# Kernel optimization log

Hardware: AMD Instinct MI355X
Metric: run time of the kernel (lower is better)

## Reference

```python
import jax, jax.numpy as jnp
import numpy as np

B, T_SRC, T_TGT = 2048, 32, 32
D = 512            # d_model
D_SRC, D_TGT = 100, 80
L = 2              # n_layers


def setup_inputs() -> dict:
    key = jax.random.key(0)
    ks = jax.random.split(key, 16)
    s = 1.0 / float(np.sqrt(D))  # torch LSTM init scale
    u = lambda k, shape: jax.random.uniform(k, shape, jnp.float32, -s, s)
    return {
        "src": jax.random.randint(ks[0], (B, T_SRC), 0, D_SRC, dtype=jnp.int32),
        "tgt": jax.random.randint(ks[1], (B, T_TGT), 0, D_TGT, dtype=jnp.int32),
        "enc_emb": jax.random.normal(ks[2], (D_SRC, D), jnp.float32),
        "dec_emb": jax.random.normal(ks[3], (D_TGT, D), jnp.float32),
        "enc_Wih": u(ks[4], (L, 4 * D, D)),
        "enc_Whh": u(ks[5], (L, 4 * D, D)),
        "enc_bih": u(ks[6], (L, 4 * D)),
        "enc_bhh": u(ks[7], (L, 4 * D)),
        "dec_Wih": u(ks[8], (L, 4 * D, D)),
        "dec_Whh": u(ks[9], (L, 4 * D, D)),
        "dec_bih": u(ks[10], (L, 4 * D)),
        "dec_bhh": u(ks[11], (L, 4 * D)),
        "post_W": u(ks[12], (D_TGT, D)),
        "post_b": u(ks[13], (D_TGT,)),
    }


def lstm_cell(x, h, c, Wih, Whh, bih, bhh):
    # PyTorch gate order: i, f, g, o
    gates = x @ Wih.T + bih + h @ Whh.T + bhh  # [B, 4D]
    i, f, g, o = jnp.split(gates, 4, axis=-1)
    c_new = jax.nn.sigmoid(f) * c + jax.nn.sigmoid(i) * jnp.tanh(g)
    h_new = jax.nn.sigmoid(o) * jnp.tanh(c_new)
    return h_new, c_new


def reference(src, tgt, enc_emb, dec_emb, enc_Wih, enc_Whh, enc_bih, enc_bhh,
              dec_Wih, dec_Whh, dec_bih, dec_bhh, post_W, post_b):
    # Eval-mode forward: dropout = identity, teacher forcing disabled
    # (tf = random() < ratio AND self.training is False at inference).
    n_layers = enc_Wih.shape[0]
    Bb = src.shape[0]
    Dm = enc_emb.shape[1]

    # ---- encoder: multi-layer LSTM over src embeddings ----
    x = enc_emb[src].swapaxes(0, 1)  # [T_src, B, D]
    hs, cs = [], []
    z = jnp.zeros((Bb, Dm), x.dtype)
    for l in range(n_layers):
        def step(carry, xt, l=l):
            h, c = carry
            h, c = lstm_cell(xt, h, c, enc_Wih[l], enc_Whh[l], enc_bih[l], enc_bhh[l])
            return (h, c), h
        (hT, cT), x = jax.lax.scan(step, (z, z), x)
        hs.append(hT)
        cs.append(cT)
    h0 = jnp.stack(hs)  # [L, B, D]
    c0 = jnp.stack(cs)  # [L, B, D]

    prev0 = dec_emb[tgt[:, 0]]  # [B, D]

    def dec_step(carry, _):
        h, c, prev = carry
        x = prev
        new_h, new_c = [], []
        for l in range(n_layers):
            hl, cl = lstm_cell(x, h[l], c[l], dec_Wih[l], dec_Whh[l], dec_bih[l], dec_bhh[l])
            new_h.append(hl)
            new_c.append(cl)
            x = hl
        logits = x @ post_W.T + post_b          # [B, d_tgt]
        pred = jnp.argmax(logits, axis=-1)       # [B]
        prev = dec_emb[pred]                     # [B, D]
        return (jnp.stack(new_h), jnp.stack(new_c), prev), logits

    _, out = jax.lax.scan(dec_step, (h0, c0, prev0), None, length=tgt.shape[1])
    return out.swapaxes(0, 1)  # [B, T_tgt, d_tgt]
```

## Files before the change

### kernel.cpp

```cpp
#include <hip/hip_runtime.h>
#include <hip/hip_bf16.h>

#define B_  2048
#define T_  32
#define D_  512
#define G_  2048
#define VT_ 80
#define BD  (B_ * D_)
#define LWE ((size_t)G_ * D_)

typedef _Float16 half8 __attribute__((ext_vector_type(8)));
typedef _Float16 half4_t __attribute__((ext_vector_type(4)));
typedef float    f32x4 __attribute__((ext_vector_type(4)));

static __device__ __forceinline__ float sigm(float x) {
    return 1.0f / (1.0f + expf(-x));
}

__global__ void zero_ws(int4* __restrict__ p, int n) {
    int i = blockIdx.x * blockDim.x + threadIdx.x;
    if (i < n) p[i] = int4{0, 0, 0, 0};
}
__global__ void init_pred(const int* __restrict__ tgt, int* __restrict__ pred) {
    int i = blockIdx.x * blockDim.x + threadIdx.x;
    if (i < B_) pred[i] = tgt[i * T_];
}

__global__ void split_weights(const float* __restrict__ s0, const float* __restrict__ s1,
                              const float* __restrict__ s2, const float* __restrict__ s3,
                              const float* __restrict__ s4, const float* __restrict__ s5,
                              _Float16* __restrict__ Wbase) {
    int g = blockIdx.x * blockDim.x + threadIdx.x;
    int mat = g >> 17;
    int rem = g & 131071;
    int np  = rem >> 6;
    int kq  = rem & 63;
    const float* src = (mat == 0) ? s0 : (mat == 1) ? s1 : (mat == 2) ? s2
                     : (mat == 3) ? s3 : (mat == 4) ? s4 : s5;
    int n = (np & 3) * D_ + (np >> 2);
    const float* sp = src + (size_t)n * D_ + kq * 8;
    float4 v0 = ((const float4*)sp)[0], v1 = ((const float4*)sp)[1];
    float x[8] = {v0.x, v0.y, v0.z, v0.w, v1.x, v1.y, v1.z, v1.w};
    _Float16 hi[8], lo[8];
    #pragma unroll
    for (int u = 0; u < 8; ++u) {
        hi[u] = (_Float16)x[u];
        lo[u] = (_Float16)(x[u] - (float)hi[u]);
    }
    int tile = (np >> 4) * 16 + (kq >> 2);
    int lane = (np & 15) | ((kq & 3) << 4);
    size_t e = (size_t)tile * 512 + (size_t)lane * 8;
    _Float16* Whi = Wbase + (size_t)mat * (2 * LWE);
    _Float16* Wlo = Whi + LWE;
    *(half8*)(Whi + e) = *(half8*)hi;
    *(half8*)(Wlo + e) = *(half8*)lo;
}

__global__ void split_postW(const float* __restrict__ pw,
                            _Float16* __restrict__ Ph, _Float16* __restrict__ Pl) {
    int g = blockIdx.x * blockDim.x + threadIdx.x;
    if (g >= VT_ * 64) return;
    int v = g >> 6, kq = g & 63;
    const float* sp = pw + (size_t)v * D_ + kq * 8;
    float4 v0 = ((const float4*)sp)[0], v1 = ((const float4*)sp)[1];
    float x[8] = {v0.x, v0.y, v0.z, v0.w, v1.x, v1.y, v1.z, v1.w};
    _Float16 hi[8], lo[8];
    #pragma unroll
    for (int u = 0; u < 8; ++u) {
        hi[u] = (_Float16)x[u];
        lo[u] = (_Float16)(x[u] - (float)hi[u]);
    }
    int tile = (v >> 4) * 16 + (kq >> 2);
    int lane = (v & 15) | ((kq & 3) << 4);
    size_t e = (size_t)tile * 512 + (size_t)lane * 8;
    *(half8*)(Ph + e) = *(half8*)hi;
    *(half8*)(Pl + e) = *(half8*)lo;
}

__global__ void perm_bias(const float* __restrict__ ebih, const float* __restrict__ ebhh,
                          const float* __restrict__ dbih, const float* __restrict__ dbhh,
                          float* __restrict__ biasP) {
    int i = blockIdx.x * blockDim.x + threadIdx.x;
    int cfg = i >> 11, np = i & 2047;
    int n = (np & 3) * D_ + (np >> 2);
    const float* bi = ((cfg < 2) ? ebih : dbih) + (cfg & 1) * G_;
    const float* bh = ((cfg < 2) ? ebhh : dbhh) + (cfg & 1) * G_;
    biasP[cfg * G_ + np] = bi[n] + bh[n];
}

__global__ __launch_bounds__(256) void compute_P(
    const float* __restrict__ enc_emb, const float* __restrict__ dec_emb,
    const float* __restrict__ encW0,   const float* __restrict__ decW0,
    float* __restrict__ P) {
    __shared__ float es[10][D_];
    __shared__ float part[4][64][10];
    int by = blockIdx.y;
    bool enc = (by < 10);
    int r0 = enc ? by * 10 : 100 + (by - 10) * 10;
    int s0 = enc ? by * 10 : (by - 10) * 10;
    const float* emb = enc ? enc_emb : dec_emb;
    const float* W   = enc ? encW0 : decW0;
    int tid = threadIdx.x;
    #pragma unroll
    for (int it = 0; it < 5; ++it) {
        int i4 = it * 256 + tid;
        int rr = i4 >> 7, cc = i4 & 127;
        ((float4*)es[rr])[cc] = ((const float4*)(emb + (size_t)(s0 + rr) * D_))[cc];
    }
    __syncthreads();
    int o   = tid & 63;
    int seg = tid >> 6;
    int np = blockIdx.x * 64 + o;
    int n = (np & 3) * D_ + (np >> 2);
    const float* wr = W + (size_t)n * D_ + seg * 128;
    float acc[10];
    #pragma unroll
    for (int rr = 0; rr < 10; ++rr) acc[rr] = 0.f;
    for (int k = 0; k < 128; k += 4) {
        float4 w4 = *(const float4*)(wr + k);
        int kb = seg * 128 + k;
        #pragma unroll
        for (int rr = 0; rr < 10; ++rr)
            acc[rr] += es[rr][kb] * w4.x + es[rr][kb+1] * w4.y
                     + es[rr][kb+2] * w4.z + es[rr][kb+3] * w4.w;
    }
    #pragma unroll
    for (int rr = 0; rr < 10; ++rr) part[seg][o][rr] = acc[rr];
    __syncthreads();
    for (int i = tid; i < 640; i += 256) {
        int o2 = i & 63, rr = i >> 6;
        P[(size_t)(r0 + rr) * G_ + blockIdx.x * 64 + o2] =
            (part[0][o2][rr] + part[1][o2][rr]) + (part[2][o2][rr] + part[3][o2][rr]);
    }
}

static __device__ __forceinline__ void load_chunk(
    const _Float16* __restrict__ Ah, const _Float16* __restrict__ Al,
    const _Float16* __restrict__ Wh, const _Float16* __restrict__ Wl,
    int afr, int wfr, int kc, int lane, half8* A8, half8* B8) {
    size_t lo8 = (size_t)lane * 8;
    #pragma unroll
    for (int i = 0; i < 4; ++i) {
        size_t off = (((size_t)(afr + i) * 16 + kc) << 9) + lo8;
        A8[i]     = *(const half8*)(Ah + off);
        A8[4 + i] = *(const half8*)(Al + off);
    }
    #pragma unroll
    for (int j = 0; j < 4; ++j) {
        size_t off = (((size_t)(wfr + j) * 16 + kc) << 9) + lo8;
        B8[j]     = *(const half8*)(Wh + off);
        B8[4 + j] = *(const half8*)(Wl + off);
    }
}
static __device__ __forceinline__ void mfma_chunk(
    const half8* A8, const half8* B8, f32x4 acc[4][4]) {
    #pragma unroll
    for (int i = 0; i < 4; ++i)
        #pragma unroll
        for (int j = 0; j < 4; ++j) {
            acc[i][j] = __builtin_amdgcn_mfma_f32_16x16x32_f16(A8[i], B8[j], acc[i][j], 0, 0, 0);
            acc[i][j] = __builtin_amdgcn_mfma_f32_16x16x32_f16(A8[i], B8[4 + j], acc[i][j], 0, 0, 0);
            acc[i][j] = __builtin_amdgcn_mfma_f32_16x16x32_f16(A8[4 + i], B8[j], acc[i][j], 0, 0, 0);
        }
}

struct CellJob {
    const _Float16 *a0h, *a0l, *w0h, *w0l;
    int kclo0, kchi0;
    const _Float16 *a1h, *a1l, *w1h, *w1l;
    int kclo1, kchi1;
    const float *biasP;
    const float *P;
    const int  *idx;
    int idx_stride, emb_rows;
    float *c_io;
    _Float16 *hh_out, *hl_out;
};

__global__ __launch_bounds__(512, 2) void lstm_cell_mfma(CellJob J0, CellJob J1) {
    const CellJob J = (blockIdx.z == 0) ? J0 : J1;
    __shared__ float gf[128][68];
    const int tid  = threadIdx.x;
    const int w    = tid >> 6;
    const int lane = tid & 63;
    const int g    = w >> 2;
    const int mw   = w & 3;
    const int id   = blockIdx.x;
    const int bx   = id >> 3;
    const int m0   = (id & 7) * 256;

    const _Float16* Ah = g ? J.a1h : J.a0h;
    const _Float16* Al = g ? J.a1l : J.a0l;
    const _Float16* Wh = g ? J.w1h : J.w0h;
    const _Float16* Wl = g ? J.w1l : J.w0l;
    const int kclo = g ? J.kclo1 : J.kclo0;
    const int kchi = g ? J.kchi1 : J.kchi0;

    const int afr = (m0 >> 4) + mw * 4;
    const int wfr = bx * 4;

    f32x4 acc[4][4];
    #pragma unroll
    for (int i = 0; i < 4; ++i)
        #pragma unroll
        for (int j = 0; j < 4; ++j) acc[i][j] = f32x4{0.f, 0.f, 0.f, 0.f};

    half8 A0[8], B0[8], A1[8], B1[8];
    load_chunk(Ah, Al, Wh, Wl, afr, wfr, kclo, lane, A0, B0);
    for (int kc = kclo; kc < kchi; kc += 2) {
        load_chunk(Ah, Al, Wh, Wl, afr, wfr, kc + 1, lane, A1, B1);
        mfma_chunk(A0, B0, acc);
        if (kc + 2 < kchi)
            load_chunk(Ah, Al, Wh, Wl, afr, wfr, kc + 2, lane, A0, B0);
        mfma_chunk(A1, B1, acc);
    }

    const int rbase = (lane >> 4) << 2;
    const int cbase = lane & 15;
    for (int p = 0; p < 2; ++p) {
        if (g == 0 && (mw >> 1) == p) {
            #pragma unroll
            for (int i = 0; i < 4; ++i) {
                int mrow = (mw & 1) * 64 + i * 16 + rbase;
                #pragma unroll
                for (int j = 0; j < 4; ++j) {
                    int nc = j * 16 + cbase;
                    #pragma unroll
                    for (int r = 0; r < 4; ++r)
                        gf[mrow + r][nc] = acc[i][j][r];
                }
            }
        }
        __syncthreads();
        if (g == 1 && (mw >> 1) == p) {
            #pragma unroll
            for (int i = 0; i < 4; ++i) {
                int mrow = (mw & 1) * 64 + i * 16 + rbase;
                #pragma unroll
                for (int j = 0; j < 4; ++j) {
                    int nc = j * 16 + cbase;
                    #pragma unroll
                    for (int r = 0; r < 4; ++r)
                        gf[mrow + r][nc] += acc[i][j][r];
                }
            }
        }
        __syncthreads();
        {
            int mr = tid >> 2, q = tid & 3;
            int mg = m0 + p * 128 + mr;
            const float4* brow = (const float4*)(J.biasP + (bx << 6));
            const float4* Pr = nullptr;
            if (J.P) {
                int s = J.idx[mg * J.idx_stride];
                s = min(max(s, 0), J.emb_rows - 1);
                Pr = (const float4*)(J.P + (size_t)s * G_ + (bx << 6));
            }
            float* crow = J.c_io + (size_t)mg * D_ + (bx << 4) + (q << 2);
            float4 cv = *(float4*)crow;
            _Float16 hh4[4], hl4[4];
            #pragma unroll
            for (int e = 0; e < 4; ++e) {
                int dl = (q << 2) + e;
                float4 g4 = *(float4*)&gf[mr][dl << 2];
                float4 b4 = brow[dl];
                float gi = g4.x + b4.x, gF = g4.y + b4.y;
                float gg = g4.z + b4.z, go = g4.w + b4.w;
                if (Pr) {
                    float4 p4 = Pr[dl];
                    gi += p4.x; gF += p4.y; gg += p4.z; go += p4.w;
                }
                float cc = (&cv.x)[e];
                float cn = sigm(gF) * cc + sigm(gi) * tanhf(gg);
                float hn = sigm(go) * tanhf(cn);
                (&cv.x)[e] = cn;
                _Float16 hH = (_Float16)hn;
                hh4[e] = hH;
                hl4[e] = (_Float16)(hn - (float)hH);
            }
            *(float4*)crow = cv;
            int kk = (bx << 4) + (q << 2);
            size_t hoff = ((size_t)((mg >> 4) * 16 + (kk >> 5)) << 9)
                        + (size_t)((mg & 15) | (((kk >> 3) & 3) << 4)) * 8
                        + ((q & 1) << 2);
            *(half4_t*)(J.hh_out + hoff) = *(half4_t*)hh4;
            *(half4_t*)(J.hl_out + hoff) = *(half4_t*)hl4;
        }
        __syncthreads();
    }
}

__global__ __launch_bounds__(128) void logits_mfma(
    const _Float16* __restrict__ Ah, const _Float16* __restrict__ Al,
    const _Float16* __restrict__ Bh, const _Float16* __restrict__ Bl,
    const float* __restrict__ postb, float* __restrict__ out,
    int t, int* __restrict__ pred) {
    __shared__ float gf2[64][85];
    __shared__ float pb[VT_];
    const int tid = threadIdx.x;
    const int w = tid >> 6;
    const int lane = tid & 63;
    const int m0 = blockIdx.x * 64;
    const int afr = blockIdx.x * 4;

    f32x4 acc[4][5];
    #pragma unroll
    for (int i = 0; i < 4; ++i)
        #pragma unroll
        for (int j = 0; j < 5; ++j) acc[i][j] = f32x4{0.f, 0.f, 0.f, 0.f};

    size_t lo8 = (size_t)lane * 8;
    for (int kc = w * 8; kc < w * 8 + 8; ++kc) {
        half8 A8[8], Bh8[5], Bl8[5];
        #pragma unroll
        for (int i = 0; i < 4; ++i) {
            size_t off = (((size_t)(afr + i) * 16 + kc) << 9) + lo8;
            A8[i]     = *(const half8*)(Ah + off);
            A8[4 + i] = *(const half8*)(Al + off);
        }
        #pragma unroll
        for (int j = 0; j < 5; ++j) {
            size_t off = (((size_t)(j * 16 + kc)) << 9) + lo8;
            Bh8[j] = *(const half8*)(Bh + off);
            Bl8[j] = *(const half8*)(Bl + off);
        }
        #pragma unroll
        for (int i = 0; i < 4; ++i)
            #pragma unroll
            for (int j = 0; j < 5; ++j) {
                acc[i][j] = __builtin_amdgcn_mfma_f32_16x16x32_f16(A8[i], Bh8[j], acc[i][j], 0, 0, 0);
                acc[i][j] = __builtin_amdgcn_mfma_f32_16x16x32_f16(A8[i], Bl8[j], acc[i][j], 0, 0, 0);
                acc[i][j] = __builtin_amdgcn_mfma_f32_16x16x32_f16(A8[4 + i], Bh8[j], acc[i][j], 0, 0, 0);
            }
    }

    if (tid < VT_) pb[tid] = postb[tid];
    const int quad = lane >> 4, c = lane & 15;
    if (w == 0) {
        #pragma unroll
        for (int i = 0; i < 4; ++i)
            #pragma unroll
            for (int j = 0; j < 5; ++j)
                #pragma unroll
                for (int r = 0; r < 4; ++r)
                    gf2[i * 16 + quad * 4 + r][j * 16 + c] = acc[i][j][r];
    }
    __syncthreads();
    if (w == 1) {
        #pragma unroll
        for (int i = 0; i < 4; ++i)
            #pragma unroll
            for (int j = 0; j < 5; ++j)
                #pragma unroll
                for (int r = 0; r < 4; ++r)
                    gf2[i * 16 + quad * 4 + r][j * 16 + c] += acc[i][j][r];
    }
    __syncthreads();
    if (tid < 64) {
        int r = tid;
        float best = -3.4e38f; int bi = 0;
        #pragma unroll
        for (int v = 0; v < VT_; ++v) {
            float x = gf2[r][v] + pb[v];
            if (x > best) { best = x; bi = v; }
        }
        pred[m0 + r] = bi;
        float* orow = out + (size_t)(m0 + r) * (T_ * VT_) + (size_t)t * VT_;
        #pragma unroll
        for (int v4 = 0; v4 < VT_ / 4; ++v4) {
            float4 g4 = *(float4*)&gf2[r][v4 * 4];
            float4 b4 = *(float4*)&pb[v4 * 4];
            float4 o4 = {g4.x + b4.x, g4.y + b4.y, g4.z + b4.z, g4.w + b4.w};
            *(float4*)(orow + v4 * 4) = o4;
        }
    }
}

extern "C" void kernel_launch(void* const* d_in, const int* in_sizes, int n_in,
                              void* d_out, int out_size, void* d_ws, size_t ws_size,
                              hipStream_t stream) {
    (void)in_sizes; (void)n_in; (void)out_size; (void)ws_size;

    const int*   src     = (const int*)d_in[0];
    const int*   tgt     = (const int*)d_in[1];
    const float* enc_emb = (const float*)d_in[2];
    const float* dec_emb = (const float*)d_in[3];
    const float* enc_Wih = (const float*)d_in[4];
    const float* enc_Whh = (const float*)d_in[5];
    const float* enc_bih = (const float*)d_in[6];
    const float* enc_bhh = (const float*)d_in[7];
    const float* dec_Wih = (const float*)d_in[8];
    const float* dec_Whh = (const float*)d_in[9];
    const float* dec_bih = (const float*)d_in[10];
    const float* dec_bhh = (const float*)d_in[11];
    const float* post_W  = (const float*)d_in[12];
    const float* post_b  = (const float*)d_in[13];

    char* wsb = (char*)d_ws;
    int*   pred  = (int*)wsb;
    float* biasB = (float*)(wsb + 16384);
    float* Ptab  = (float*)(wsb + 16384 + 32768);
    char*  zbase = wsb + 16384 + 32768 + 180 * G_ * 4;
    float* C0 = (float*)zbase;
    float* C1 = C0 + BD;
    _Float16* Hh00 = (_Float16*)(C1 + BD);
    _Float16* Hh10 = Hh00 + BD;
    _Float16* Hl00 = Hh10 + BD;
    _Float16* Hl10 = Hl00 + BD;
    _Float16* Hh01 = Hl10 + BD;
    _Float16* Hh11 = Hh01 + BD;
    _Float16* Hl01 = Hh11 + BD;
    _Float16* Hl11 = Hl01 + BD;
    _Float16* Wb   = Hl11 + BD;
    _Float16* PwH  = Wb + 6 * 2 * LWE;
    _Float16* PwL  = PwH + (size_t)VT_ * D_;

    _Float16* Hhi[2][2] = { { Hh00, Hh01 }, { Hh10, Hh11 } };
    _Float16* Hlo[2][2] = { { Hl00, Hl01 }, { Hl10, Hl11 } };
    float*    Cp[2]     = { C0, C1 };
    auto WP = [&](int m, int pl) { return Wb + (size_t)m * (2 * LWE) + (size_t)pl * LWE; };

    float* out = (float*)d_out;

    zero_ws<<<4096, 256, 0, stream>>>((int4*)zbase, (16 * 1024 * 1024) / 16);
    init_pred<<<8, 256, 0, stream>>>(tgt, pred);
    split_weights<<<3072, 256, 0, stream>>>(
        enc_Whh, enc_Wih + LWE, enc_Whh + LWE,
        dec_Whh, dec_Wih + LWE, dec_Whh + LWE, Wb);
    split_postW<<<20, 256, 0, stream>>>(post_W, PwH, PwL);
    perm_bias<<<32, 256, 0, stream>>>(enc_bih, enc_bhh, dec_bih, dec_bhh, biasB);
    {
        dim3 gP(32, 18);
        compute_P<<<gP, 256, 0, stream>>>(enc_emb, dec_emb, enc_Wih, dec_Wih, Ptab);
    }

    dim3 grid1(256, 1, 1);
    dim3 grid2(256, 1, 2);
    int c0 = 0, c1 = 0;

    auto mkL0 = [&](bool enc, const int* ix, int stride, int rows) {
        int m = enc ? 0 : 3;
        CellJob j;
        j.a0h = Hhi[0][c0]; j.a0l = Hlo[0][c0];
        j.w0h = WP(m, 0);   j.w0l = WP(m, 1);
        j.kclo0 = 0; j.kchi0 = 8;
        j.a1h = Hhi[0][c0]; j.a1l = Hlo[0][c0];
        j.w1h = WP(m, 0);   j.w1l = WP(m, 1);
        j.kclo1 = 8; j.kchi1 = 16;
        j.biasP = biasB + (enc ? 0 : 2) * G_;
        j.P = enc ? Ptab : Ptab + (size_t)100 * G_;
        j.idx = ix; j.idx_stride = stride; j.emb_rows = rows;
        j.c_io = Cp[0];
        j.hh_out = Hhi[0][c0 ^ 1]; j.hl_out = Hlo[0][c0 ^ 1];
        return j;
    };
    auto mkL1 = [&](bool enc) {
        int mi = enc ? 1 : 4, mh = enc ? 2 : 5;
        CellJob j;
        j.a0h = Hhi[0][c0]; j.a0l = Hlo[0][c0];
        j.w0h = WP(mi, 0);  j.w0l = WP(mi, 1);
        j.kclo0 = 0; j.kchi0 = 16;
        j.a1h = Hhi[1][c1]; j.a1l = Hlo[1][c1];
        j.w1h = WP(mh, 0);  j.w1l = WP(mh, 1);
        j.kclo1 = 0; j.kchi1 = 16;
        j.biasP = biasB + (enc ? 1 : 3) * G_;
        j.P = nullptr; j.idx = nullptr; j.idx_stride = 0; j.emb_rows = 0;
        j.c_io = Cp[1];
        j.hh_out = Hhi[1][c1 ^ 1]; j.hl_out = Hlo[1][c1 ^ 1];
        return j;
    };

    {
        CellJob j0 = mkL0(true, src + 0, T_, 100);
        lstm_cell_mfma<<<grid1, 512, 0, stream>>>(j0, j0);
        c0 ^= 1;
        for (int t = 0; t < T_ - 1; ++t) {
            CellJob jA = mkL1(true);
            CellJob jB = mkL0(true, src + t + 1, T_, 100);
            lstm_cell_mfma<<<grid2, 512, 0, stream>>>(jA, jB);
            c1 ^= 1; c0 ^= 1;
        }
        CellJob jZ = mkL1(true);
        lstm_cell_mfma<<<grid1, 512, 0, stream>>>(jZ, jZ);
        c1 ^= 1;
    }

    for (int t = 0; t < T_; ++t) {
        CellJob j0 = mkL0(false, pred, 1, VT_);
        lstm_cell_mfma<<<grid1, 512, 0, stream>>>(j0, j0);
        c0 ^= 1;
        CellJob j1 = mkL1(false);
        lstm_cell_mfma<<<grid1, 512, 0, stream>>>(j1, j1);
        c1 ^= 1;
        logits_mfma<<<32, 128, 0, stream>>>(
            Hhi[1][c1], Hlo[1][c1], PwH, PwL, post_b, out, t, pred);
    }
}
```

Measured before the change: 4.287 ms.

## Stage LSTM weight tiles into LDS with async global_load_lds ring buffer

The weight (B operand) fragments are no longer loaded by every warp into registers. They are now fetched with global_load_lds into a 4-deep shared-memory ring that the two K-split warp groups share. Each warp stages one weight tile, the loop is unrolled by four with s_waitcnt/barrier synchronisation, and the A operand stays in registers with double buffering. The goal is to cut redundant global weight traffic and register pressure and to overlap loads with MFMA. In exchange it adds a block-wide barrier per K chunk, uses 64KB of LDS, and assumes (kchi-kclo) is divisible by 4.

```diff
diff --git a/kernel.cpp b/kernel.cpp
--- a/kernel.cpp
+++ b/kernel.cpp
@@ -16,6 +16,20 @@
 static __device__ __forceinline__ float sigm(float x) {
     return 1.0f / (1.0f + expf(-x));
 }
+
+typedef __attribute__((address_space(1))) unsigned int gas_u32;
+typedef __attribute__((address_space(3))) unsigned int las_u32;
+static __device__ __forceinline__ void glds16(const void* src, void* dst) {
+    __builtin_amdgcn_global_load_lds(
+        (gas_u32*)(unsigned long long)(size_t)src,
+        (las_u32*)(unsigned int)(size_t)dst, 16, 0, 0);
+}
+
+#define WB() do {                                         \
+    asm volatile("s_waitcnt vmcnt(2)" ::: "memory");      \
+    __builtin_amdgcn_s_barrier();                         \
+    __builtin_amdgcn_sched_barrier(0);                    \
+} while (0)
 
 __global__ void zero_ws(int4* __restrict__ p, int n) {
     int i = blockIdx.x * blockDim.x + threadIdx.x;
@@ -134,36 +148,6 @@
     }
 }
 
-static __device__ __forceinline__ void load_chunk(
-    const _Float16* __restrict__ Ah, const _Float16* __restrict__ Al,
-    const _Float16* __restrict__ Wh, const _Float16* __restrict__ Wl,
-    int afr, int wfr, int kc, int lane, half8* A8, half8* B8) {
-    size_t lo8 = (size_t)lane * 8;
-    #pragma unroll
-    for (int i = 0; i < 4; ++i) {
-        size_t off = (((size_t)(afr + i) * 16 + kc) << 9) + lo8;
-        A8[i]     = *(const half8*)(Ah + off);
-        A8[4 + i] = *(const half8*)(Al + off);
-    }
-    #pragma unroll
-    for (int j = 0; j < 4; ++j) {
-        size_t off = (((size_t)(wfr + j) * 16 + kc) << 9) + lo8;
-        B8[j]     = *(const half8*)(Wh + off);
-        B8[4 + j] = *(const half8*)(Wl + off);
-    }
-}
-static __device__ __forceinline__ void mfma_chunk(
-    const half8* A8, const half8* B8, f32x4 acc[4][4]) {
-    #pragma unroll
-    for (int i = 0; i < 4; ++i)
-        #pragma unroll
-        for (int j = 0; j < 4; ++j) {
-            acc[i][j] = __builtin_amdgcn_mfma_f32_16x16x32_f16(A8[i], B8[j], acc[i][j], 0, 0, 0);
-            acc[i][j] = __builtin_amdgcn_mfma_f32_16x16x32_f16(A8[i], B8[4 + j], acc[i][j], 0, 0, 0);
-            acc[i][j] = __builtin_amdgcn_mfma_f32_16x16x32_f16(A8[4 + i], B8[j], acc[i][j], 0, 0, 0);
-        }
-}
-
 struct CellJob {
     const _Float16 *a0h, *a0l, *w0h, *w0l;
     int kclo0, kchi0;
@@ -179,7 +163,9 @@
 
 __global__ __launch_bounds__(512, 2) void lstm_cell_mfma(CellJob J0, CellJob J1) {
     const CellJob J = (blockIdx.z == 0) ? J0 : J1;
-    __shared__ float gf[128][68];
+    __shared__ __align__(128) char smem[65536];
+    float (*gf)[68] = (float (*)[68])smem;
+
     const int tid  = threadIdx.x;
     const int w    = tid >> 6;
     const int lane = tid & 63;
@@ -205,14 +191,74 @@
         #pragma unroll
         for (int j = 0; j < 4; ++j) acc[i][j] = f32x4{0.f, 0.f, 0.f, 0.f};
 
-    half8 A0[8], B0[8], A1[8], B1[8];
-    load_chunk(Ah, Al, Wh, Wl, afr, wfr, kclo, lane, A0, B0);
-    for (int kc = kclo; kc < kchi; kc += 2) {
-        load_chunk(Ah, Al, Wh, Wl, afr, wfr, kc + 1, lane, A1, B1);
-        mfma_chunk(A0, B0, acc);
-        if (kc + 2 < kchi)
-            load_chunk(Ah, Al, Wh, Wl, afr, wfr, kc + 2, lane, A0, B0);
-        mfma_chunk(A1, B1, acc);
+    char* const sb = smem + w * 2048;
+    const char* const rg0 = smem + (g << 13);
+
+    auto stage = [&](int buf, int kc) {
+        size_t toff = (((size_t)(wfr + (w & 3)) * 16 + kc) << 9) + (size_t)lane * 8;
+        char* d = sb + buf * 16384;
+        glds16(Wh + toff, d);
+        glds16(Wl + toff, d + 1024);
+    };
+    auto ldA = [&](half8* A8, int kc) {
+        size_t lo8 = (size_t)lane * 8;
+        #pragma unroll
+        for (int i = 0; i < 4; ++i) {
+            size_t off = (((size_t)(afr + i) * 16 + kc) << 9) + lo8;
+            A8[i]     = *(const half8*)(Ah + off);
+            A8[4 + i] = *(const half8*)(Al + off);
+        }
+    };
+    auto domfma = [&](const half8* A8, int buf) {
+        const char* r = rg0 + buf * 16384;
+        size_t lo16 = (size_t)lane * 16;
+        #pragma unroll
+        for (int j = 0; j < 4; ++j) {
+            half8 Bh = *(const half8*)(r + j * 2048 + lo16);
+            half8 Bl = *(const half8*)(r + j * 2048 + 1024 + lo16);
+            #pragma unroll
+            for (int i = 0; i < 4; ++i) {
+                acc[i][j] = __builtin_amdgcn_mfma_f32_16x16x32_f16(A8[i], Bh, acc[i][j], 0, 0, 0);
+                acc[i][j] = __builtin_amdgcn_mfma_f32_16x16x32_f16(A8[i], Bl, acc[i][j], 0, 0, 0);
+                acc[i][j] = __builtin_amdgcn_mfma_f32_16x16x32_f16(A8[4 + i], Bh, acc[i][j], 0, 0, 0);
+            }
+        }
+    };
+
+    half8 A0[8], A1[8];
+    const int nit = (kchi - kclo) >> 2;
+
+    ldA(A0, kclo);
+    __builtin_amdgcn_sched_barrier(0);
+    stage(0, kclo);
+    stage(1, kclo + 1);
+    WB();
+
+    for (int it = 0; it < nit; ++it) {
+        const int k0 = kclo + (it << 2);
+        const bool more = (it + 1 < nit);
+
+        ldA(A1, k0 + 1); __builtin_amdgcn_sched_barrier(0);
+        stage(2, k0 + 2);
+        domfma(A0, 0);
+        WB();
+
+        ldA(A0, k0 + 2); __builtin_amdgcn_sched_barrier(0);
+        stage(3, k0 + 3);
+        domfma(A1, 1);
+        WB();
+
+        ldA(A1, k0 + 3); __builtin_amdgcn_sched_barrier(0);
+        if (more) stage(0, k0 + 4);
+        domfma(A0, 2);
+        WB();
+
+        if (more) {
+            ldA(A0, k0 + 4); __builtin_amdgcn_sched_barrier(0);
+            stage(1, k0 + 5);
+        }
+        domfma(A1, 3);
+        WB();
     }
 
     const int rbase = (lane >> 4) << 2;
```

After: 4.273 ms. No clear change (-0.3%).
